# Kernel optimization log

Hardware: AMD Instinct MI355X
Metric: run time of the kernel (lower is better)

The kernel has to match this reference:

```python
import jax, jax.numpy as jnp
import numpy as np

EPS = 1.1920929e-7  # torch.finfo(float32).eps, default for F.rms_norm
ATTN_SCALE = 0.1
ROPE_BASE = 10000.0


def _rms_norm(x):
    # F.rms_norm over last dim, no learned weight
    return x * jax.lax.rsqrt(jnp.mean(x * x, axis=-1, keepdims=True) + EPS)


def _rotary(x):
    # x: [B, T, H, D]; rotates halves as in the Rotary module
    T, D = x.shape[1], x.shape[3]
    half = D // 2
    inv_freq = 1.0 / (ROPE_BASE ** (jnp.arange(0, D, 2, dtype=jnp.float32) / D))  # [half]
    freqs = jnp.arange(T, dtype=jnp.float32)[:, None] * inv_freq[None, :]          # [T, half]
    cos = jnp.cos(freqs)[None, :, None, :]
    sin = jnp.sin(freqs)[None, :, None, :]
    x1, x2 = x[..., :half], x[..., half:]
    return jnp.concatenate([x1 * cos + x2 * sin, -x1 * sin + x2 * cos], axis=-1)


def setup_inputs() -> dict:
    key = jax.random.key(0)
    ks = jax.random.split(key, 8)
    B, T, dim, H, hd = 2, 2048, 1024, 16, 64
    gate_in = 12
    s = 1.0 / np.sqrt(dim)
    return {
        "x": jax.random.normal(ks[0], (B, T, dim), dtype=jnp.float32),
        "v1": jax.random.normal(ks[1], (B, T, H, hd), dtype=jnp.float32),
        "Wq": jax.random.uniform(ks[2], (dim, dim), jnp.float32, -s, s),
        "Wk": jax.random.uniform(ks[3], (dim, dim), jnp.float32, -s, s),
        "Wv": jax.random.uniform(ks[4], (dim, dim), jnp.float32, -s, s),
        "Wproj": jax.random.uniform(ks[5], (dim, dim), jnp.float32, -s, s),
        "Wg": jax.random.uniform(ks[6], (H, gate_in), jnp.float32,
                                  -1.0 / np.sqrt(gate_in), 1.0 / np.sqrt(gate_in)),
        "lamb": jnp.float32(0.5),
    }


def reference(x, v1, Wq, Wk, Wv, Wproj, Wg, lamb):
    B, T, dim = x.shape
    H, hd = v1.shape[2], v1.shape[3]
    q = (x @ Wq.T).reshape(B, T, H, hd)
    k = (x @ Wk.T).reshape(B, T, H, hd)
    v = (x @ Wv.T).reshape(B, T, H, hd)
    # value-residual mixing
    v = (1.0 - lamb) * v + lamb * v1
    # QK RMSNorm + RoPE
    q = _rotary(_rms_norm(q))
    k = _rotary(_rms_norm(k))
    # causal SDPA with fixed scale
    scores = jnp.einsum('bqhd,bkhd->bhqk', q, k) * ATTN_SCALE
    causal = jnp.tril(jnp.ones((T, T), dtype=bool))
    scores = jnp.where(causal[None, None], scores, jnp.float32(-jnp.inf))
    probs = jax.nn.softmax(scores, axis=-1)
    y = jnp.einsum('bhqk,bkhd->bqhd', probs, v)  # [B, T, H, hd]
    # sigmoid gate from first 12 channels of x
    gate = jax.nn.sigmoid(x[..., :Wg.shape[1]] @ Wg.T)  # [B, T, H]
    y = y * gate[..., None]
    y = y.reshape(B, T, H * hd) @ Wproj.T
    return y
```

## Files before the change

kernel.cpp:

```cpp
#include <hip/hip_runtime.h>
#include <math.h>


#define B_    2
#define T_    2048
#define DIM_  1024
#define H_    16
#define HD_   64
#define NROW  (B_ * T_)
#define EPS_  1.1920929e-07f
#define SCALE_ 0.1f
#define LOG2_10K 13.287712379549449f
#define INV2PI 0.15915494309189535f

typedef unsigned short u16;
typedef unsigned int   u32;
typedef __bf16 bf16x8 __attribute__((ext_vector_type(8)));
typedef __bf16 bf16x2 __attribute__((ext_vector_type(2)));
typedef float  f32x4  __attribute__((ext_vector_type(4)));

__device__ __forceinline__ u16 f2b(float f) {
  u32 u = __float_as_uint(f);
  u += 0x7fffu + ((u >> 16) & 1u);
  return (u16)(u >> 16);
}
__device__ __forceinline__ u32 pk2(float a, float b) {
#if __has_builtin(__builtin_amdgcn_cvt_pk_bf16_f32)
  bf16x2 r = __builtin_amdgcn_cvt_pk_bf16_f32(a, b);
  return __builtin_bit_cast(u32, r);
#else
  return (u32)f2b(a) | ((u32)f2b(b) << 16);
#endif
}
__device__ __forceinline__ void fast_sincos_rev(float rev, float* s, float* c) {
  const float r = rev - floorf(rev);
#if __has_builtin(__builtin_amdgcn_sinf) && __has_builtin(__builtin_amdgcn_cosf)
  *s = __builtin_amdgcn_sinf(r);
  *c = __builtin_amdgcn_cosf(r);
#else
  *s = __sinf(r * 6.283185307179586f);
  *c = __cosf(r * 6.283185307179586f);
#endif
}
#define MFMA16(a,b,c) __builtin_amdgcn_mfma_f32_16x16x32_bf16((a),(b),(c),0,0,0)

typedef const __attribute__((address_space(1))) unsigned char gbuf_t;
typedef __attribute__((address_space(3))) unsigned char lbuf_t;
__device__ __forceinline__ void gload_lds16(const u16* g, unsigned char* l) {
  __builtin_amdgcn_global_load_lds((gbuf_t*)g, (lbuf_t*)l, 16, 0, 0);
}

__global__ __launch_bounds__(256) void convert_all(
    const float* __restrict__ x, const float* __restrict__ Wq,
    const float* __restrict__ Wk, const float* __restrict__ Wv,
    const float* __restrict__ Wp,
    u16* __restrict__ xb, u16* __restrict__ wb) {
  const int i = blockIdx.x * 256 + threadIdx.x;
  if (i < 1835008) {
    const float* src; u16* dst; int off;
    if (i < 1048576)      { src = x;  dst = xb;           off = i; }
    else if (i < 1310720) { src = Wq; dst = wb;           off = i - 1048576; }
    else if (i < 1572864) { src = Wk; dst = wb + 1048576; off = i - 1310720; }
    else                  { src = Wv; dst = wb + 2097152; off = i - 1572864; }
    const float4 f = ((const float4*)src)[off];
    uint2 o;
    o.x = pk2(f.x, f.y);
    o.y = pk2(f.z, f.w);
    ((uint2*)dst)[off] = o;
  } else {
    const int off = i - 1835008;
    const int blk = off >> 6, ln = off & 63;
    const int row = ((blk >> 5) << 4) + (ln & 15);
    const int col = ((blk & 31) << 5) + ((ln >> 4) << 3);
    const float4 f0 = *(const float4*)(Wp + (size_t)row * DIM_ + col);
    const float4 f1 = *(const float4*)(Wp + (size_t)row * DIM_ + col + 4);
    uint4 o;
    o.x = pk2(f0.x, f0.y); o.y = pk2(f0.z, f0.w);
    o.z = pk2(f1.x, f1.y); o.w = pk2(f1.z, f1.w);
    ((uint4*)(wb + 3145728))[off] = o;
  }
}

__global__ __launch_bounds__(256) void gemm_qkv(
    const u16* __restrict__ Ab, const u16* __restrict__ Wb,
    u16* __restrict__ qo, u16* __restrict__ ko, u16* __restrict__ vto,
    const float* __restrict__ v1, const float* __restrict__ lambp) {
  __shared__ __attribute__((aligned(16))) unsigned char sm[49152];
  const int tid  = threadIdx.x;
  const int w    = tid >> 6;
  const int lane = tid & 63;
  const int lo = lane & 15, hi = lane >> 4;
  const int m0 = blockIdx.x << 7;
  const int by = blockIdx.y;
  const int mode = by >> 3;
  const int n0 = (by & 7) << 7;
  const u16* W = Wb + (size_t)mode * (DIM_ * DIM_);
  const int wm = w & 1, wn = w >> 1;

  const u16* agA0 = Ab + (size_t)(m0 + (2 * w + 0) * 16 + lo) * DIM_ + (hi << 3);
  const u16* agA1 = Ab + (size_t)(m0 + (2 * w + 1) * 16 + lo) * DIM_ + (hi << 3);
  const u16* agB0 = W  + (size_t)(n0 + (2 * w + 0) * 16 + lo) * DIM_ + (hi << 3);
  const u16* agB1 = W  + (size_t)(n0 + (2 * w + 1) * 16 + lo) * DIM_ + (hi << 3);

  f32x4 acc[4][4];
#pragma unroll
  for (int i = 0; i < 4; ++i)
#pragma unroll
    for (int j = 0; j < 4; ++j) acc[i][j] = (f32x4){0.f, 0.f, 0.f, 0.f};

  {
    unsigned char* ad0 = sm + (2 * w) * 1024;
    gload_lds16(agA0, ad0);
    gload_lds16(agA1, ad0 + 1024);
    gload_lds16(agB0, ad0 + 8192);
    gload_lds16(agB1, ad0 + 9216);
    agA0 += 32; agA1 += 32; agB0 += 32; agB1 += 32;
    unsigned char* ad1 = sm + 16384 + (2 * w) * 1024;
    gload_lds16(agA0, ad1);
    gload_lds16(agA1, ad1 + 1024);
    gload_lds16(agB0, ad1 + 8192);
    gload_lds16(agB1, ad1 + 9216);
    agA0 += 32; agA1 += 32; agB0 += 32; agB1 += 32;
  }

  int cr = 0, cw = 2;
  for (int kc = 0; kc < DIM_; kc += 32) {
    __builtin_amdgcn_sched_barrier(0);
    if (kc + 32 < DIM_) {
      asm volatile("s_waitcnt vmcnt(4)" ::: "memory");
    } else {
      asm volatile("s_waitcnt vmcnt(0)" ::: "memory");
    }
    __builtin_amdgcn_s_barrier();
    __builtin_amdgcn_sched_barrier(0);
    if (kc + 64 < DIM_) {
      unsigned char* ad = sm + cw * 16384 + (2 * w) * 1024;
      gload_lds16(agA0, ad);
      gload_lds16(agA1, ad + 1024);
      gload_lds16(agB0, ad + 8192);
      gload_lds16(agB1, ad + 9216);
      agA0 += 32; agA1 += 32; agB0 += 32; agB1 += 32;
    }
    const unsigned char* Acur = sm + cr * 16384;
    const unsigned char* Bcur = Acur + 8192;
    bf16x8 bfr[4];
#pragma unroll
    for (int nt = 0; nt < 4; ++nt)
      bfr[nt] = *(const bf16x8*)(Bcur + (((wn * 4 + nt) * 64 + lane) << 4));
#pragma unroll
    for (int mt = 0; mt < 4; ++mt) {
      const bf16x8 af = *(const bf16x8*)(Acur + (((wm * 4 + mt) * 64 + lane) << 4));
#pragma unroll
      for (int nt = 0; nt < 4; ++nt)
        acc[mt][nt] = MFMA16(af, bfr[nt], acc[mt][nt]);
    }
    cr = (cr == 2) ? 0 : cr + 1;
    cw = (cw == 2) ? 0 : cw + 1;
  }

  const int head = (n0 >> 6) + wn;
  if (mode <= 1) {
    u16* C = (mode == 0) ? qo : ko;
    const float if0 = exp2f(-(float)lo * (LOG2_10K / 32.f)) * INV2PI;
    const float if1 = exp2f(-(float)(lo + 16) * (LOG2_10K / 32.f)) * INV2PI;
#pragma unroll
    for (int mt = 0; mt < 4; ++mt)
#pragma unroll
      for (int r = 0; r < 4; ++r) {
        float ss = 0.f;
#pragma unroll
        for (int nt = 0; nt < 4; ++nt) { const float v = acc[mt][nt][r]; ss += v * v; }
        ss += __shfl_xor(ss, 1, 64); ss += __shfl_xor(ss, 2, 64);
        ss += __shfl_xor(ss, 4, 64); ss += __shfl_xor(ss, 8, 64);
        const float scl = rsqrtf(ss * (1.f / 64.f) + EPS_);
        const int row_g = m0 + wm * 64 + mt * 16 + hi * 4 + r;
        const float tpos = (float)(row_g & (T_ - 1));
        float sn0, cs0, sn1, cs1;
        fast_sincos_rev(tpos * if0, &sn0, &cs0);
        fast_sincos_rev(tpos * if1, &sn1, &cs1);
        u16* crow = C + (size_t)row_g * DIM_ + head * HD_;
        const float x10 = acc[mt][0][r] * scl, x11 = acc[mt][1][r] * scl;
        const float x20 = acc[mt][2][r] * scl, x21 = acc[mt][3][r] * scl;
        crow[lo]      = f2b(x10 * cs0 + x20 * sn0);
        crow[16 + lo] = f2b(x11 * cs1 + x21 * sn1);
        crow[32 + lo] = f2b(x20 * cs0 - x10 * sn0);
        crow[48 + lo] = f2b(x21 * cs1 - x11 * sn1);
      }
  } else {
    const float lam = lambp[0];
#pragma unroll
    for (int mt = 0; mt < 4; ++mt)
#pragma unroll
      for (int r = 0; r < 4; ++r) {
        const int row_g = m0 + wm * 64 + mt * 16 + hi * 4 + r;
        const int bb = row_g >> 11, tt = row_g & (T_ - 1);
        const int bh = bb * H_ + head;
        const float* v1r = v1 + (size_t)row_g * DIM_ + head * HD_;
#pragma unroll
        for (int nt = 0; nt < 4; ++nt) {
          const int d = nt * 16 + lo;
          const float ov = (1.f - lam) * acc[mt][nt][r] + lam * v1r[d];
          vto[((size_t)(bh * HD_ + d)) * T_ + tt] = f2b(ov);
        }
      }
  }
}

__global__ __launch_bounds__(256) void gemm_proj(
    const u16* __restrict__ Ab, const u16* __restrict__ Wb,
    float* __restrict__ fo) {
  const int tid  = threadIdx.x;
  const int w    = tid >> 6;
  const int lane = tid & 63;
  const int lo = lane & 15, hi = lane >> 4;
  const int raw = blockIdx.x;
  const int xcd = raw & 7;
  const int jj  = raw >> 3;
  const int m0 = (xcd * 4 + (jj & 3)) << 7;
  const int n0 = (jj >> 2) << 7;
  const int wm = w & 1, wn = w >> 1;

  const u16* pA = Ab + (size_t)((m0 >> 4) + wm * 4) * 16384 + lane * 8;
  const u16* pB = Wb + (size_t)((n0 >> 4) + wn * 4) * 16384 + lane * 8;

  f32x4 acc[4][4];
#pragma unroll
  for (int i = 0; i < 4; ++i)
#pragma unroll
    for (int j = 0; j < 4; ++j) acc[i][j] = (f32x4){0.f, 0.f, 0.f, 0.f};

  bf16x8 aE[4], bE[4], aO[4], bO[4];
#pragma unroll
  for (int t = 0; t < 4; ++t) {
    aE[t] = *(const bf16x8*)(pA + t * 16384);
    bE[t] = *(const bf16x8*)(pB + t * 16384);
  }
  for (int ks = 0; ks < 32; ks += 2) {
#pragma unroll
    for (int t = 0; t < 4; ++t) {
      aO[t] = *(const bf16x8*)(pA + t * 16384 + (ks + 1) * 512);
      bO[t] = *(const bf16x8*)(pB + t * 16384 + (ks + 1) * 512);
    }
#pragma unroll
    for (int mt = 0; mt < 4; ++mt)
#pragma unroll
      for (int nt = 0; nt < 4; ++nt)
        acc[mt][nt] = MFMA16(aE[mt], bE[nt], acc[mt][nt]);
    const int kn = (ks + 2 < 32) ? (ks + 2) : 0;
#pragma unroll
    for (int t = 0; t < 4; ++t) {
      aE[t] = *(const bf16x8*)(pA + t * 16384 + kn * 512);
      bE[t] = *(const bf16x8*)(pB + t * 16384 + kn * 512);
    }
#pragma unroll
    for (int mt = 0; mt < 4; ++mt)
#pragma unroll
      for (int nt = 0; nt < 4; ++nt)
        acc[mt][nt] = MFMA16(aO[mt], bO[nt], acc[mt][nt]);
  }

#pragma unroll
  for (int mt = 0; mt < 4; ++mt)
#pragma unroll
    for (int r = 0; r < 4; ++r) {
      const int row_g = m0 + wm * 64 + mt * 16 + hi * 4 + r;
      float* orow = fo + (size_t)row_g * DIM_ + n0 + wn * 64;
#pragma unroll
      for (int nt = 0; nt < 4; ++nt) orow[nt * 16 + lo] = acc[mt][nt][r];
    }
}

__global__ __launch_bounds__(256) void gate_kernel(
    const float* __restrict__ x, const float* __restrict__ Wg,
    float* __restrict__ gate) {
  const int id = blockIdx.x * 256 + threadIdx.x;
  const int n = id >> 4, h = id & 15;
  const float* xr = x + (size_t)n * DIM_;
  const float* wr = Wg + h * 12;
  float s = 0.f;
#pragma unroll
  for (int j = 0; j < 12; ++j) s += xr[j] * wr[j];
  gate[id] = 1.f / (1.f + __expf(-s));
}

__global__ __launch_bounds__(256) void attn3(
    const u16* __restrict__ q, const u16* __restrict__ k, const u16* __restrict__ vt,
    const float* __restrict__ gate, u16* __restrict__ yt) {
  __shared__ __attribute__((aligned(16))) unsigned char smem[49152];
  const int tid = threadIdx.x;
  const int wv = tid >> 6, lane = tid & 63, lo = lane & 15, hi = lane >> 4;
  const int raw = blockIdx.x;
  const int xcd = raw & 7;
  const int jj  = raw >> 3;
  const int qt = 31 - (jj >> 2);
  const int bh = xcd * 4 + (jj & 3);
  const int b = bh >> 4, h = bh & 15;
  const int qb = qt << 6;

  const int qrow = b * T_ + qb + wv * 16 + lo;
  const u16* qp = q + (size_t)qrow * DIM_ + h * HD_;
  const bf16x8 qf0 = *(const bf16x8*)(qp + hi * 8);
  const bf16x8 qf1 = *(const bf16x8*)(qp + 32 + hi * 8);

  f32x4 o[4];
#pragma unroll
  for (int i = 0; i < 4; ++i) o[i] = (f32x4){0.f, 0.f, 0.f, 0.f};
  float lrun = 0.f;

  const int sl = tid & 63, skh = (tid >> 6) & 1, st0 = tid >> 7;
  const int srow = sl & 15, skk = skh * 32 + ((sl >> 4) << 3);
  const u16* kg0 = k + ((size_t)(b * T_ + st0 * 16 + srow)) * DIM_ + h * HD_ + skk;
  const u16* kg1 = kg0 + (size_t)32 * DIM_;
  const u16* vg0 = vt + ((size_t)(bh * HD_ + st0 * 16 + srow)) * T_ + skk;
  const u16* vg1 = vg0 + (size_t)32 * T_;
  const int wub = (tid >> 6) << 10;

  {
    gload_lds16(kg0, smem + wub);
    gload_lds16(kg1, smem + 4096 + wub);
    gload_lds16(vg0, smem + 8192 + wub);
    gload_lds16(vg1, smem + 12288 + wub);
    const int t1 = (qt >= 1) ? 1 : 0;
    const size_t ko = (size_t)t1 * 64 * DIM_;
    const size_t vo = (size_t)t1 * 64;
    unsigned char* b1 = smem + 16384;
    gload_lds16(kg0 + ko, b1 + wub);
    gload_lds16(kg1 + ko, b1 + 4096 + wub);
    gload_lds16(vg0 + vo, b1 + 8192 + wub);
    gload_lds16(vg1 + vo, b1 + 12288 + wub);
  }

  int sr = 0, sw = 2;
  for (int tix = 0; tix <= qt; ++tix) {
    __builtin_amdgcn_sched_barrier(0);
    if (tix < qt) {
      asm volatile("s_waitcnt vmcnt(4)" ::: "memory");
    } else {
      asm volatile("s_waitcnt vmcnt(0)" ::: "memory");
    }
    __builtin_amdgcn_s_barrier();
    __builtin_amdgcn_sched_barrier(0);
    if (tix + 2 <= qt) {
      const size_t ko = (size_t)(tix + 2) * 64 * DIM_;
      const size_t vo = (size_t)(tix + 2) * 64;
      unsigned char* base = smem + sw * 16384;
      gload_lds16(kg0 + ko, base + wub);
      gload_lds16(kg1 + ko, base + 4096 + wub);
      gload_lds16(vg0 + vo, base + 8192 + wub);
      gload_lds16(vg1 + vo, base + 12288 + wub);
    }
    const unsigned char* kb = smem + sr * 16384;
    const unsigned char* vb = kb + 8192;

    f32x4 stl[4];
#pragma unroll
    for (int kt = 0; kt < 4; ++kt) stl[kt] = (f32x4){0.f, 0.f, 0.f, 0.f};
    __builtin_amdgcn_s_setprio(1);
#pragma unroll
    for (int kh = 0; kh < 2; ++kh) {
      const bf16x8 qb_ = kh ? qf1 : qf0;
#pragma unroll
      for (int kt = 0; kt < 4; ++kt) {
        const bf16x8 af = *(const bf16x8*)(kb + (((kt * 2 + kh) * 64 + lane) << 4));
        stl[kt] = MFMA16(af, qb_, stl[kt]);
      }
    }
    __builtin_amdgcn_s_setprio(0);
    const bool diag = (tix == qt);
    float ps = 0.f;
#pragma unroll
    for (int kt = 0; kt < 4; ++kt)
#pragma unroll
      for (int r = 0; r < 4; ++r) {
        float s = stl[kt][r] * SCALE_;
        if (diag && (kt * 16 + hi * 4 + r > wv * 16 + lo)) s = -3e38f;
        const float e = __expf(s);
        stl[kt][r] = e;
        ps += e;
      }
    ps += __shfl_xor(ps, 16, 64);
    ps += __shfl_xor(ps, 32, 64);
    lrun += ps;

    u32 pkv[4][2];
#pragma unroll
    for (int kt = 0; kt < 4; ++kt) {
      pkv[kt][0] = pk2(stl[kt][0], stl[kt][1]);
      pkv[kt][1] = pk2(stl[kt][2], stl[kt][3]);
    }
#pragma unroll
    for (int kh = 0; kh < 2; ++kh) {
      uint4 w4;
      u32* w4p = (u32*)&w4;
#pragma unroll
      for (int wd = 0; wd < 4; ++wd) {
        const int src = (2 * (hi & 1) + (wd >> 1)) * 16 + lo;
        const u32 a  = (u32)__shfl((int)pkv[2 * kh][wd & 1], src, 64);
        const u32 bb = (u32)__shfl((int)pkv[2 * kh + 1][wd & 1], src, 64);
        w4p[wd] = (hi < 2) ? a : bb;
      }
      const bf16x8 pf = __builtin_bit_cast(bf16x8, w4);
      __builtin_amdgcn_s_setprio(1);
#pragma unroll
      for (int dt = 0; dt < 4; ++dt) {
        const bf16x8 vf = *(const bf16x8*)(vb + (((dt * 2 + kh) * 64 + lane) << 4));
        o[dt] = MFMA16(vf, pf, o[dt]);
      }
      __builtin_amdgcn_s_setprio(0);
    }
    sr = (sr == 2) ? 0 : sr + 1;
    sw = (sw == 2) ? 0 : sw + 1;
  }

  const float inv = gate[(size_t)qrow * H_ + h] / lrun;
  u16* ybase = yt + (size_t)(qrow >> 4) * 16384 + (size_t)(h * 2) * 512
             + lo * 8 + (hi & 1) * 4;
#pragma unroll
  for (int dt = 0; dt < 4; ++dt) {
    ushort4 pq;
    pq.x = f2b(o[dt][0] * inv); pq.y = f2b(o[dt][1] * inv);
    pq.z = f2b(o[dt][2] * inv); pq.w = f2b(o[dt][3] * inv);
    const int c = (dt * 2 + (hi >> 1)) & 3;
    *(ushort4*)(ybase + (dt >> 1) * 512 + c * 128) = pq;
  }
}

extern "C" void kernel_launch(void* const* d_in, const int* in_sizes, int n_in,
                              void* d_out, int out_size, void* d_ws, size_t ws_size,
                              hipStream_t stream) {
  const float* x    = (const float*)d_in[0];
  const float* v1   = (const float*)d_in[1];
  const float* Wq   = (const float*)d_in[2];
  const float* Wk   = (const float*)d_in[3];
  const float* Wv   = (const float*)d_in[4];
  const float* Wp   = (const float*)d_in[5];
  const float* Wg   = (const float*)d_in[6];
  const float* lamb = (const float*)d_in[7];

  const size_t NX = (size_t)NROW * DIM_;
  const size_t NW = (size_t)DIM_ * DIM_;

  u16* q  = (u16*)d_ws;
  u16* k  = q + NX;
  u16* vt = k + NX;
  u16* xb = vt + NX;
  u16* wb = xb + NX;
  float* gate = (float*)(wb + 4 * NW);

  const dim3 bb(256);

  convert_all<<<dim3(7680), bb, 0, stream>>>(x, Wq, Wk, Wv, Wp, xb, wb);
  gemm_qkv<<<dim3(32, 24), bb, 0, stream>>>(xb, wb, q, k, vt, v1, lamb);
  gate_kernel<<<dim3(NROW * H_ / 256), bb, 0, stream>>>(x, Wg, gate);
  attn3<<<dim3(1024), bb, 0, stream>>>(q, k, vt, gate, xb);
  gemm_proj<<<dim3(256), bb, 0, stream>>>(xb, wb + 3 * NW, (float*)d_out);
}
```

Before: 220.7 us.

## Double attention query tile to 128 rows per block, reusing K/V tiles

Each attention block now handles 128 query rows instead of 64, with every wave computing two 16-row query sub-tiles (A and B) against the same K/V tile held in LDS. This halves the global-to-LDS K/V traffic per query and the grid size, and the causal mask is generalised to a per-row offset. In exchange it uses more registers per wave, launches fewer blocks (512) so occupancy and load balance across CUs may suffer, and the diagonal tiles do more masked work.

```diff
diff --git a/kernel.cpp b/kernel.cpp
--- a/kernel.cpp
+++ b/kernel.cpp
@@ -292,20 +292,28 @@
   const int raw = blockIdx.x;
   const int xcd = raw & 7;
   const int jj  = raw >> 3;
-  const int qt = 31 - (jj >> 2);
+  const int qtb = 15 - (jj >> 2);
   const int bh = xcd * 4 + (jj & 3);
   const int b = bh >> 4, h = bh & 15;
-  const int qb = qt << 6;
-
-  const int qrow = b * T_ + qb + wv * 16 + lo;
-  const u16* qp = q + (size_t)qrow * DIM_ + h * HD_;
-  const bf16x8 qf0 = *(const bf16x8*)(qp + hi * 8);
-  const bf16x8 qf1 = *(const bf16x8*)(qp + 32 + hi * 8);
-
-  f32x4 o[4];
-#pragma unroll
-  for (int i = 0; i < 4; ++i) o[i] = (f32x4){0.f, 0.f, 0.f, 0.f};
-  float lrun = 0.f;
+  const int qb = qtb << 7;
+  const int nIterM1 = 2 * qtb + 1;
+
+  const int qrowA = b * T_ + qb + wv * 32 + lo;
+  const int qrowB = qrowA + 16;
+  const u16* qpA = q + (size_t)qrowA * DIM_ + h * HD_;
+  const u16* qpB = q + (size_t)qrowB * DIM_ + h * HD_;
+  const bf16x8 qfA0 = *(const bf16x8*)(qpA + hi * 8);
+  const bf16x8 qfA1 = *(const bf16x8*)(qpA + 32 + hi * 8);
+  const bf16x8 qfB0 = *(const bf16x8*)(qpB + hi * 8);
+  const bf16x8 qfB1 = *(const bf16x8*)(qpB + 32 + hi * 8);
+
+  f32x4 oA[4], oB[4];
+#pragma unroll
+  for (int i = 0; i < 4; ++i) {
+    oA[i] = (f32x4){0.f, 0.f, 0.f, 0.f};
+    oB[i] = (f32x4){0.f, 0.f, 0.f, 0.f};
+  }
+  float lrunA = 0.f, lrunB = 0.f;
 
   const int sl = tid & 63, skh = (tid >> 6) & 1, st0 = tid >> 7;
   const int srow = sl & 15, skk = skh * 32 + ((sl >> 4) << 3);
@@ -320,27 +328,24 @@
     gload_lds16(kg1, smem + 4096 + wub);
     gload_lds16(vg0, smem + 8192 + wub);
     gload_lds16(vg1, smem + 12288 + wub);
-    const int t1 = (qt >= 1) ? 1 : 0;
-    const size_t ko = (size_t)t1 * 64 * DIM_;
-    const size_t vo = (size_t)t1 * 64;
     unsigned char* b1 = smem + 16384;
-    gload_lds16(kg0 + ko, b1 + wub);
-    gload_lds16(kg1 + ko, b1 + 4096 + wub);
-    gload_lds16(vg0 + vo, b1 + 8192 + wub);
-    gload_lds16(vg1 + vo, b1 + 12288 + wub);
+    gload_lds16(kg0 + (size_t)64 * DIM_, b1 + wub);
+    gload_lds16(kg1 + (size_t)64 * DIM_, b1 + 4096 + wub);
+    gload_lds16(vg0 + 64, b1 + 8192 + wub);
+    gload_lds16(vg1 + 64, b1 + 12288 + wub);
   }
 
   int sr = 0, sw = 2;
-  for (int tix = 0; tix <= qt; ++tix) {
+  for (int tix = 0; tix <= nIterM1; ++tix) {
     __builtin_amdgcn_sched_barrier(0);
-    if (tix < qt) {
+    if (tix < nIterM1) {
       asm volatile("s_waitcnt vmcnt(4)" ::: "memory");
     } else {
       asm volatile("s_waitcnt vmcnt(0)" ::: "memory");
     }
     __builtin_amdgcn_s_barrier();
     __builtin_amdgcn_sched_barrier(0);
-    if (tix + 2 <= qt) {
+    if (tix + 2 <= nIterM1) {
       const size_t ko = (size_t)(tix + 2) * 64 * DIM_;
       const size_t vo = (size_t)(tix + 2) * 64;
       unsigned char* base = smem + sw * 16384;
@@ -352,59 +357,80 @@
     const unsigned char* kb = smem + sr * 16384;
     const unsigned char* vb = kb + 8192;
 
-    f32x4 stl[4];
-#pragma unroll
-    for (int kt = 0; kt < 4; ++kt) stl[kt] = (f32x4){0.f, 0.f, 0.f, 0.f};
+    f32x4 stlA[4], stlB[4];
+#pragma unroll
+    for (int kt = 0; kt < 4; ++kt) {
+      stlA[kt] = (f32x4){0.f, 0.f, 0.f, 0.f};
+      stlB[kt] = (f32x4){0.f, 0.f, 0.f, 0.f};
+    }
     __builtin_amdgcn_s_setprio(1);
 #pragma unroll
     for (int kh = 0; kh < 2; ++kh) {
-      const bf16x8 qb_ = kh ? qf1 : qf0;
+      const bf16x8 qA_ = kh ? qfA1 : qfA0;
+      const bf16x8 qB_ = kh ? qfB1 : qfB0;
 #pragma unroll
       for (int kt = 0; kt < 4; ++kt) {
         const bf16x8 af = *(const bf16x8*)(kb + (((kt * 2 + kh) * 64 + lane) << 4));
-        stl[kt] = MFMA16(af, qb_, stl[kt]);
+        stlA[kt] = MFMA16(af, qA_, stlA[kt]);
+        stlB[kt] = MFMA16(af, qB_, stlB[kt]);
       }
     }
     __builtin_amdgcn_s_setprio(0);
-    const bool diag = (tix == qt);
-    float ps = 0.f;
+
+    const int dq = qb + wv * 32 - tix * 64;
+    float psA = 0.f, psB = 0.f;
 #pragma unroll
     for (int kt = 0; kt < 4; ++kt)
 #pragma unroll
       for (int r = 0; r < 4; ++r) {
-        float s = stl[kt][r] * SCALE_;
-        if (diag && (kt * 16 + hi * 4 + r > wv * 16 + lo)) s = -3e38f;
-        const float e = __expf(s);
-        stl[kt][r] = e;
-        ps += e;
-      }
-    ps += __shfl_xor(ps, 16, 64);
-    ps += __shfl_xor(ps, 32, 64);
-    lrun += ps;
-
-    u32 pkv[4][2];
+        const int kl = kt * 16 + hi * 4 + r;
+        float sA = stlA[kt][r] * SCALE_;
+        float sB = stlB[kt][r] * SCALE_;
+        if (kl > dq + lo)      sA = -3e38f;
+        if (kl > dq + 16 + lo) sB = -3e38f;
+        const float eA = __expf(sA);
+        const float eB = __expf(sB);
+        stlA[kt][r] = eA; psA += eA;
+        stlB[kt][r] = eB; psB += eB;
+      }
+    psA += __shfl_xor(psA, 16, 64);
+    psA += __shfl_xor(psA, 32, 64);
+    psB += __shfl_xor(psB, 16, 64);
+    psB += __shfl_xor(psB, 32, 64);
+    lrunA += psA;
+    lrunB += psB;
+
+    u32 pkvA[4][2], pkvB[4][2];
 #pragma unroll
     for (int kt = 0; kt < 4; ++kt) {
-      pkv[kt][0] = pk2(stl[kt][0], stl[kt][1]);
-      pkv[kt][1] = pk2(stl[kt][2], stl[kt][3]);
+      pkvA[kt][0] = pk2(stlA[kt][0], stlA[kt][1]);
+      pkvA[kt][1] = pk2(stlA[kt][2], stlA[kt][3]);
+      pkvB[kt][0] = pk2(stlB[kt][0], stlB[kt][1]);
+      pkvB[kt][1] = pk2(stlB[kt][2], stlB[kt][3]);
     }
 #pragma unroll
     for (int kh = 0; kh < 2; ++kh) {
-      uint4 w4;
-      u32* w4p = (u32*)&w4;
+      uint4 w4A, w4B;
+      u32* wpA = (u32*)&w4A;
+      u32* wpB = (u32*)&w4B;
 #pragma unroll
       for (int wd = 0; wd < 4; ++wd) {
         const int src = (2 * (hi & 1) + (wd >> 1)) * 16 + lo;
-        const u32 a  = (u32)__shfl((int)pkv[2 * kh][wd & 1], src, 64);
-        const u32 bb = (u32)__shfl((int)pkv[2 * kh + 1][wd & 1], src, 64);
-        w4p[wd] = (hi < 2) ? a : bb;
-      }
-      const bf16x8 pf = __builtin_bit_cast(bf16x8, w4);
+        const u32 aA  = (u32)__shfl((int)pkvA[2 * kh][wd & 1], src, 64);
+        const u32 bA  = (u32)__shfl((int)pkvA[2 * kh + 1][wd & 1], src, 64);
+        wpA[wd] = (hi < 2) ? aA : bA;
+        const u32 aB  = (u32)__shfl((int)pkvB[2 * kh][wd & 1], src, 64);
+        const u32 bB  = (u32)__shfl((int)pkvB[2 * kh + 1][wd & 1], src, 64);
+        wpB[wd] = (hi < 2) ? aB : bB;
+      }
+      const bf16x8 pfA = __builtin_bit_cast(bf16x8, w4A);
+      const bf16x8 pfB = __builtin_bit_cast(bf16x8, w4B);
       __builtin_amdgcn_s_setprio(1);
 #pragma unroll
       for (int dt = 0; dt < 4; ++dt) {
         const bf16x8 vf = *(const bf16x8*)(vb + (((dt * 2 + kh) * 64 + lane) << 4));
-        o[dt] = MFMA16(vf, pf, o[dt]);
+        oA[dt] = MFMA16(vf, pfA, oA[dt]);
+        oB[dt] = MFMA16(vf, pfB, oB[dt]);
       }
       __builtin_amdgcn_s_setprio(0);
     }
@@ -412,16 +438,31 @@
     sw = (sw == 2) ? 0 : sw + 1;
   }
 
-  const float inv = gate[(size_t)qrow * H_ + h] / lrun;
-  u16* ybase = yt + (size_t)(qrow >> 4) * 16384 + (size_t)(h * 2) * 512
-             + lo * 8 + (hi & 1) * 4;
-#pragma unroll
-  for (int dt = 0; dt < 4; ++dt) {
-    ushort4 pq;
-    pq.x = f2b(o[dt][0] * inv); pq.y = f2b(o[dt][1] * inv);
-    pq.z = f2b(o[dt][2] * inv); pq.w = f2b(o[dt][3] * inv);
-    const int c = (dt * 2 + (hi >> 1)) & 3;
-    *(ushort4*)(ybase + (dt >> 1) * 512 + c * 128) = pq;
+  {
+    const float inv = gate[(size_t)qrowA * H_ + h] / lrunA;
+    u16* ybase = yt + (size_t)(qrowA >> 4) * 16384 + (size_t)(h * 2) * 512
+               + lo * 8 + (hi & 1) * 4;
+#pragma unroll
+    for (int dt = 0; dt < 4; ++dt) {
+      ushort4 pq;
+      pq.x = f2b(oA[dt][0] * inv); pq.y = f2b(oA[dt][1] * inv);
+      pq.z = f2b(oA[dt][2] * inv); pq.w = f2b(oA[dt][3] * inv);
+      const int c = (dt * 2 + (hi >> 1)) & 3;
+      *(ushort4*)(ybase + (dt >> 1) * 512 + c * 128) = pq;
+    }
+  }
+  {
+    const float inv = gate[(size_t)qrowB * H_ + h] / lrunB;
+    u16* ybase = yt + (size_t)(qrowB >> 4) * 16384 + (size_t)(h * 2) * 512
+               + lo * 8 + (hi & 1) * 4;
+#pragma unroll
+    for (int dt = 0; dt < 4; ++dt) {
+      ushort4 pq;
+      pq.x = f2b(oB[dt][0] * inv); pq.y = f2b(oB[dt][1] * inv);
+      pq.z = f2b(oB[dt][2] * inv); pq.w = f2b(oB[dt][3] * inv);
+      const int c = (dt * 2 + (hi >> 1)) & 3;
+      *(ushort4*)(ybase + (dt >> 1) * 512 + c * 128) = pq;
+    }
   }
 }
 
@@ -452,6 +493,6 @@
   convert_all<<<dim3(7680), bb, 0, stream>>>(x, Wq, Wk, Wv, Wp, xb, wb);
   gemm_qkv<<<dim3(32, 24), bb, 0, stream>>>(xb, wb, q, k, vt, v1, lamb);
   gate_kernel<<<dim3(NROW * H_ / 256), bb, 0, stream>>>(x, Wg, gate);
-  attn3<<<dim3(1024), bb, 0, stream>>>(q, k, vt, gate, xb);
+  attn3<<<dim3(512), bb, 0, stream>>>(q, k, vt, gate, xb);
   gemm_proj<<<dim3(256), bb, 0, stream>>>(xb, wb + 3 * NW, (float*)d_out);
 }
```

Measured after the change: 240.7 us. 9.1% more time.
